# Optimization experiments

Measured on AMD Instinct MI355X. Metric: run time of the kernel, lower is better.

Reference implementation:

```python
import jax, jax.numpy as jnp
import numpy as np

H = 8  # heads hardcoded in LightGFormer


def layernorm(x, g, b, eps=1e-5):
    m = x.mean(-1, keepdims=True)
    v = ((x - m) ** 2).mean(-1, keepdims=True)
    return (x - m) / jnp.sqrt(v + eps) * g + b


def setup_inputs() -> dict:
    key = jax.random.key(0)
    B, N, D, L = 16, 512, 256, 4
    Dff = 4 * D
    ks = jax.random.split(key, 12)

    def w(k, shape, scale=0.02):
        return jax.random.normal(k, shape, jnp.float32) * scale

    return {
        "input": w(ks[0], (B, N, D), 1.0),
        "input_v": w(ks[1], (B, N, D), 1.0),
        "pos_emb": w(ks[2], (N, D)),
        "Wq": w(ks[3], (L, D, D)), "bq": jnp.zeros((L, D), jnp.float32),
        "Wk": w(ks[4], (L, D, D)), "bk": jnp.zeros((L, D), jnp.float32),
        "Wv": w(ks[5], (L, D, D)), "bv": jnp.zeros((L, D), jnp.float32),
        "Wo": w(ks[6], (L, D, D)), "bo": jnp.zeros((L, D), jnp.float32),
        "W1": w(ks[7], (L, D, Dff)), "b1": jnp.zeros((L, Dff), jnp.float32),
        "W2": w(ks[8], (L, Dff // 2, D // 2)), "b2": jnp.zeros((L, D // 2), jnp.float32),
        "g1": jnp.ones((L, D), jnp.float32), "be1": jnp.zeros((L, D), jnp.float32),
        "g2": jnp.ones((L, D), jnp.float32), "be2": jnp.zeros((L, D), jnp.float32),
        "gf": jnp.ones((D,), jnp.float32), "bf": jnp.zeros((D,), jnp.float32),
        "mask": jax.random.randint(ks[9], (N, N), 0, 2) > 0,
    }


def reference(input, input_v, pos_emb, Wq, bq, Wk, bk, Wv, bv, Wo, bo,
              W1, b1, W2, b2, g1, be1, g2, be2, gf, bf, mask):
    B, N, D = input.shape
    L = Wq.shape[0]
    dk = D // H
    scale = 1.0 / float(np.sqrt(dk))

    x = input + pos_emb[None]       # learned positional encoding
    xv = input_v + pos_emb[None]    # values stream (never updated across layers)

    for i in range(L):
        # --- self-attention: queries/keys from x, values from xv ---
        q = (x @ Wq[i] + bq[i]).reshape(B, N, H, dk)
        k = (x @ Wk[i] + bk[i]).reshape(B, N, H, dk)
        v = (xv @ Wv[i] + bv[i]).reshape(B, N, H, dk)
        att = jnp.einsum('bqhd,bkhd->bhqk', q, k) * scale
        if i % 2 == 1:  # odd layers use the mask (Lightformer alternation)
            att = jnp.where(mask[None, None], -jnp.inf, att)
        att = jax.nn.softmax(att, axis=-1)
        o = jnp.einsum('bhqk,bkhd->bqhd', att, v).reshape(B, N, D)
        o = o @ Wo[i] + bo[i]
        x = layernorm(x + o, g1[i], be1[i])
        # --- FFN with grouped second linear: [.., 2, 2D] @ [2D, D/2] ---
        h = jax.nn.gelu(x @ W1[i] + b1[i], approximate=False)
        h = (h.reshape(B, N, 2, 2 * D) @ W2[i] + b2[i]).reshape(B, N, D)
        x = layernorm(x + h, g2[i], be2[i])

    x = layernorm(x, gf, bf)  # final attention_norm
    return x
```

## Files before the change

### kernel.cpp

```cpp
#include <hip/hip_runtime.h>
#include <hip/hip_bf16.h>
#include <math.h>

#define BDIM 16
#define NSEQ 512
#define DMODEL 256
#define NLAYER 4
#define NHEAD 8
#define DK 32
#define DFF 1024
#define BN (BDIM * NSEQ)
#define ND (NSEQ * DMODEL)

typedef __bf16 bf16x8 __attribute__((ext_vector_type(8)));
typedef float floatx4 __attribute__((ext_vector_type(4)));
typedef unsigned uint32x2 __attribute__((ext_vector_type(2)));

static __device__ __forceinline__ unsigned short f2bf(float f) {
    unsigned u = __float_as_uint(f);
    unsigned r = (u + 0x7FFFu + ((u >> 16) & 1u)) >> 16;
    return (unsigned short)r;
}
static __device__ __forceinline__ float bf2f(unsigned short u) {
    return __uint_as_float(((unsigned)u) << 16);
}

static __device__ __forceinline__ void async_ld16(const unsigned short* g,
                                                  unsigned short* l) {
    __builtin_amdgcn_global_load_lds(
        (const __attribute__((address_space(1))) unsigned int*)g,
        (__attribute__((address_space(3))) unsigned int*)l, 16, 0, 0);
}

static __device__ __forceinline__ float gelu_f(float c) {
    float u = 0.7978845608028654f * (c + 0.044715f * c * c * c);
    return c * (1.f / (1.f + __expf(-2.f * u)));
}

static __device__ __forceinline__ unsigned cvtpk(float lo, float hi) {
    unsigned r;
    asm("v_cvt_pk_bf16_f32 %0, %1, %2" : "=v"(r) : "v"(lo), "v"(hi));
    return r;
}

static __device__ __forceinline__ size_t fd_addr(int tok, int col) {
    int panel = tok >> 4, l16 = tok & 15;
    int kt = col >> 5, kp = col & 31;
    int quad = (kp >> 2) & 3;
    int j = (kp & 3) + 4 * ((kp >> 4) & 1);
    return ((size_t)(panel * 8 + kt) << 9) + (l16 * 4 + quad) * 8 + j;
}

__global__ void conv_all_kernel(const float* __restrict__ Wq, const float* __restrict__ Wk,
                                const float* __restrict__ Wv, const float* __restrict__ Wo,
                                const float* __restrict__ W1, const float* __restrict__ W2,
                                const int* __restrict__ mask,
                                unsigned short* __restrict__ wq_s, unsigned short* __restrict__ wk_s,
                                unsigned short* __restrict__ wv_s,
                                unsigned short* __restrict__ wo_s,
                                unsigned short* __restrict__ w1_s, unsigned short* __restrict__ w2_s,
                                unsigned* __restrict__ bits) {
    int blk = blockIdx.x, tid = threadIdx.x;
    if (blk < 3072) {
        int i = blk * 256 + tid;
        int sel = i >> 18;
        int jj = i & 262143;
        int l = jj >> 16, o = jj & 65535;
        int j = o & 7, quad = (o >> 3) & 3, l16 = (o >> 5) & 15;
        int kt = (o >> 9) & 7, cg = (o >> 12) & 15;
        int k = kt * 32 + (j >> 2) * 16 + quad * 4 + (j & 3);
        int dout = cg * 16 + l16;
        const float* src = sel == 0 ? Wq : sel == 1 ? Wk : Wv;
        unsigned short* dst = sel == 0 ? wq_s : sel == 1 ? wk_s : wv_s;
        dst[(size_t)l * 65536 + o] = f2bf(src[(size_t)l * 65536 + k * 256 + dout]);
    } else if (blk < 4096) {
        int i = (blk - 3072) * 256 + tid;
        int l = i >> 16, o = i & 65535;
        int j = o & 7, quad = (o >> 3) & 3, l16 = (o >> 5) & 15;
        int kt = (o >> 9) & 7, cg = (o >> 12) & 15;
        int k = kt * 32 + (j >> 2) * 16 + quad * 4 + (j & 3);
        int dout = cg * 16 + l16;
        wo_s[(size_t)l * 65536 + o] = f2bf(Wo[(size_t)l * 65536 + k * 256 + dout]);
    } else if (blk < 8192) {
        int i = (blk - 4096) * 256 + tid;
        int l = i >> 18, o = i & 262143;
        int j = o & 7, quad = (o >> 3) & 3, l16 = (o >> 5) & 15;
        int kt = (o >> 9) & 7, cg = (o >> 12) & 63;
        int k = kt * 32 + (j >> 2) * 16 + quad * 4 + (j & 3);
        int dout = cg * 16 + l16;
        w1_s[(size_t)l * 262144 + o] = f2bf(W1[(size_t)l * 262144 + k * 1024 + dout]);
    } else if (blk < 9216) {
        int i = (blk - 8192) * 256 + tid;
        int l = i >> 16, o = i & 65535;
        int j = o & 7, quad = (o >> 3) & 3, l16 = (o >> 5) & 15;
        int kt = (o >> 9) & 15, cg = (o >> 13) & 7;
        int k = kt * 32 + (j >> 2) * 16 + quad * 4 + (j & 3);
        int dout = cg * 16 + l16;
        w2_s[(size_t)l * 65536 + o] = f2bf(W2[(size_t)l * 65536 + k * 128 + dout]);
    } else {
        int w = (blk - 9216) * 256 + tid;
        int r = w >> 4, wi = w & 15;
        const int* src = mask + r * NSEQ + wi * 32;
        unsigned acc = 0;
#pragma unroll
        for (int j = 0; j < 32; j++) acc |= (src[j] != 0 ? 1u : 0u) << j;
        bits[w] = acc;
    }
}

__global__ void add_pos_kernel(const float* __restrict__ in,
                               const float* __restrict__ inv,
                               const float* __restrict__ pos,
                               float* __restrict__ x,
                               unsigned short* __restrict__ xb,
                               unsigned short* __restrict__ xvb,
                               int total) {
    int i = blockIdx.x * blockDim.x + threadIdx.x;
    if (i < total) {
        float pe = pos[i % ND];
        float a = in[i] + pe;
        float b = inv[i] + pe;
        x[i] = a;
        size_t fa = fd_addr(i >> 8, i & 255);
        xb[fa] = f2bf(a);
        xvb[fa] = f2bf(b);
    }
}

__global__ __launch_bounds__(256) void qkv_mfma_kernel(
        const unsigned short* __restrict__ xb_f,
        const unsigned short* __restrict__ xvb_f,
        const unsigned short* __restrict__ wq_s, const unsigned short* __restrict__ wk_s,
        const unsigned short* __restrict__ wv_s,
        const float* __restrict__ bq, const float* __restrict__ bk,
        const float* __restrict__ bv,
        unsigned short* __restrict__ qo, unsigned short* __restrict__ ko,
        unsigned short* __restrict__ vo) {
    int bx = blockIdx.x;
    int proj = bx >> 9, panel = bx & 511;
    const unsigned short* A  = (proj == 2) ? xvb_f : xb_f;
    const unsigned short* W  = (proj == 0) ? wq_s : (proj == 1) ? wk_s : wv_s;
    const float* bias        = (proj == 0) ? bq  : (proj == 1) ? bk  : bv;
    unsigned short* Cb       = (proj == 0) ? qo  : (proj == 1) ? ko  : vo;
    float qscale = (proj == 0) ? 0.17677669529663687f : 1.f;

    int tid = threadIdx.x;
    int w = tid >> 6, lane = tid & 63, l16 = lane & 15, quad = lane >> 4;
    int fo = (l16 * 4 + quad) * 8;

    floatx4 acc[4];
#pragma unroll
    for (int cg = 0; cg < 4; cg++) acc[cg] = (floatx4)0.0f;

    bf16x8 afQ[4], bwQ[4][4];
#pragma unroll
    for (int p = 0; p < 4; p++) {
        afQ[p] = *(const bf16x8*)(A + ((size_t)panel * 8 + p) * 512 + fo);
#pragma unroll
        for (int cg = 0; cg < 4; cg++)
            bwQ[p][cg] = *(const bf16x8*)(W + ((size_t)((w * 4 + cg) * 8 + p)) * 512 + fo);
    }

#pragma unroll
    for (int kt = 0; kt < 8; kt++) {
        int sl = kt & 3;
#pragma unroll
        for (int cg = 0; cg < 4; cg++)
            acc[cg] = __builtin_amdgcn_mfma_f32_16x16x32_bf16(afQ[sl], bwQ[sl][cg], acc[cg], 0, 0, 0);
        if (kt < 4) {
            afQ[sl] = *(const bf16x8*)(A + ((size_t)panel * 8 + kt + 4) * 512 + fo);
#pragma unroll
            for (int cg = 0; cg < 4; cg++)
                bwQ[sl][cg] = *(const bf16x8*)(W + ((size_t)((w * 4 + cg) * 8 + kt + 4)) * 512 + fo);
        }
    }

#pragma unroll
    for (int cg = 0; cg < 4; cg++) {
        int gcol = w * 64 + cg * 16 + l16;
        float bb = bias[gcol];
#pragma unroll
        for (int r = 0; r < 4; r++) {
            int grow = panel * 16 + quad * 4 + r;
            float c = (acc[cg][r] + bb) * qscale;
            size_t off = ((size_t)((grow >> 9) * 8 + (gcol >> 5)) << 14)
                       + (size_t)(grow & 511) * 32 + (gcol & 31);
            Cb[off] = f2bf(c);
        }
    }
}

__global__ __launch_bounds__(512, 4) void ffn_fused_kernel(
        const unsigned short* __restrict__ ab_f,
        const unsigned short* __restrict__ wo_s,
        const unsigned short* __restrict__ w1_s,
        const unsigned short* __restrict__ w2_s,
        const float* __restrict__ bo,
        const float* __restrict__ g1, const float* __restrict__ be1,
        const float* __restrict__ b1,
        const float* __restrict__ b2,
        const float* __restrict__ g2, const float* __restrict__ be2,
        const float* __restrict__ gf, const float* __restrict__ bf_,
        float* __restrict__ xf, unsigned short* __restrict__ xb,
        float* __restrict__ outF, int finalize) {
    __shared__ unsigned short X1s[8 * 512];
    __shared__ unsigned short Hs[16 * 512];
    __shared__ float redA[16][8], redB[16][8];
    __shared__ float redC[16][8], redD[16][8];
    __shared__ float redE[16][8], redF[16][8];

    int tid = threadIdx.x;
    int w = tid >> 6, lane = tid & 63, l16 = lane & 15, quad = lane >> 4;
    int bid = blockIdx.x;
    int rowBase = bid * 16;
    int fo = (l16 * 4 + quad) * 8;

#define TR2(d0, d1, addr)                                                  \
    asm volatile("ds_read_b64_tr_b16 %0, %2\n\t"                           \
                 "ds_read_b64_tr_b16 %1, %2 offset:512"                    \
                 : "=&v"(d0), "=&v"(d1) : "v"(addr))

    float bo_r[2], g1_r[2], be1_r[2], g2_r[2], be2_r[2], gf_r[2], bfr_[2];
#pragma unroll
    for (int cg = 0; cg < 2; cg++) {
        int colA = w * 32 + cg * 16 + l16;
        bo_r[cg] = bo[colA]; g1_r[cg] = g1[colA]; be1_r[cg] = be1[colA];
        int colC = cg * 128 + w * 16 + l16;
        g2_r[cg] = g2[colC]; be2_r[cg] = be2[colC];
        gf_r[cg] = gf[colC]; bfr_[cg] = bf_[colC];
    }
    float b1_r[2][4];
#pragma unroll
    for (int g = 0; g < 2; g++)
#pragma unroll
        for (int c = 0; c < 4; c++)
            b1_r[g][c] = b1[g * 512 + w * 64 + c * 16 + l16];
    float b2_r = b2[w * 16 + l16];
    float x0r[4][2];
#pragma unroll
    for (int r = 0; r < 4; r++)
#pragma unroll
        for (int cg = 0; cg < 2; cg++)
            x0r[r][cg] = xf[(size_t)(rowBase + quad * 4 + r) * 256 + w * 32 + cg * 16 + l16];

    floatx4 accA[2];
    accA[0] = (floatx4)0.0f; accA[1] = (floatx4)0.0f;

    bf16x8 afQ[4], bwQ[4][2];
#pragma unroll
    for (int p = 0; p < 4; p++) {
        afQ[p] = *(const bf16x8*)(ab_f + ((size_t)bid * 8 + p) * 512 + fo);
#pragma unroll
        for (int cg = 0; cg < 2; cg++)
            bwQ[p][cg] = *(const bf16x8*)(wo_s + ((size_t)((w * 2 + cg) * 8 + p)) * 512 + fo);
    }

#pragma unroll
    for (int kt = 0; kt < 8; kt++) {
        int sl = kt & 3;
#pragma unroll
        for (int cg = 0; cg < 2; cg++)
            accA[cg] = __builtin_amdgcn_mfma_f32_16x16x32_bf16(afQ[sl], bwQ[sl][cg], accA[cg], 0, 0, 0);
        if (kt < 4) {
            afQ[sl] = *(const bf16x8*)(ab_f + ((size_t)bid * 8 + kt + 4) * 512 + fo);
#pragma unroll
            for (int cg = 0; cg < 2; cg++)
                bwQ[sl][cg] = *(const bf16x8*)(wo_s + ((size_t)((w * 2 + cg) * 8 + kt + 4)) * 512 + fo);
        }
    }

#pragma unroll
    for (int r = 0; r < 4; r++) {
        int tok = quad * 4 + r;
        float s = 0.f, s2 = 0.f;
#pragma unroll
        for (int cg = 0; cg < 2; cg++) {
            float v = accA[cg][r] + bo_r[cg] + x0r[r][cg];
            accA[cg][r] = v; s += v; s2 += v * v;
        }
#pragma unroll
        for (int off = 1; off <= 8; off <<= 1) {
            s += __shfl_xor(s, off);
            s2 += __shfl_xor(s2, off);
        }
        if (l16 == 0) { redA[tok][w] = s; redB[tok][w] = s2; }
    }
    __syncthreads();
#pragma unroll
    for (int r = 0; r < 4; r++) {
        int tok = quad * 4 + r;
        float ts = 0.f, tq = 0.f;
#pragma unroll
        for (int ww = 0; ww < 8; ww++) { ts += redA[tok][ww]; tq += redB[tok][ww]; }
        float mean = ts * (1.f / 256.f);
        float var = tq * (1.f / 256.f) - mean * mean;
        float rstd = rsqrtf(var + 1e-5f);
#pragma unroll
        for (int cg = 0; cg < 2; cg++)
            accA[cg][r] = (accA[cg][r] - mean) * rstd * g1_r[cg] + be1_r[cg];
    }
#pragma unroll
    for (int cg = 0; cg < 2; cg++) {
        uint32x2 pk;
        pk[0] = cvtpk(accA[cg][0], accA[cg][1]);
        pk[1] = cvtpk(accA[cg][2], accA[cg][3]);
        *(uint32x2*)&X1s[w * 512 + (cg * 16 + l16) * 16 + quad * 4] = pk;
    }
    __syncthreads();

    unsigned x1addr = (unsigned)(size_t)&X1s[0] + (unsigned)(lane * 8);
    unsigned haddr  = (unsigned)(size_t)&Hs[0]  + (unsigned)(lane * 8);

    floatx4 y[2];
    y[0] = (floatx4)0.0f; y[1] = (floatx4)0.0f;

#pragma unroll
    for (int g = 0; g < 2; g++) {
        floatx4 accB[4];
#pragma unroll
        for (int c = 0; c < 4; c++) accB[c] = (floatx4)0.0f;

        uint32x2 tA0, tA1, tB0, tB1;
        TR2(tA0, tA1, x1addr);
        TR2(tB0, tB1, x1addr + 1024u);
        bf16x8 bwB[2][4];
#pragma unroll
        for (int p = 0; p < 2; p++)
#pragma unroll
            for (int c = 0; c < 4; c++)
                bwB[p][c] = *(const bf16x8*)(w1_s +
                    ((size_t)((g * 32 + w * 4 + c) * 8 + p)) * 512 + fo);

#pragma unroll
        for (int kt = 0; kt < 8; kt++) {
            if (kt < 7) asm volatile("s_waitcnt lgkmcnt(2)");
            else        asm volatile("s_waitcnt lgkmcnt(0)");
            __builtin_amdgcn_sched_barrier(0);
            union { bf16x8 v8; uint32x2 u[2]; } afu;
            if ((kt & 1) == 0) { afu.u[0] = tA0; afu.u[1] = tA1; }
            else               { afu.u[0] = tB0; afu.u[1] = tB1; }
            if (kt < 6) {
                if ((kt & 1) == 0) TR2(tA0, tA1, x1addr + (unsigned)((kt + 2) * 1024));
                else               TR2(tB0, tB1, x1addr + (unsigned)((kt + 2) * 1024));
            }
            int sl = kt & 1;
#pragma unroll
            for (int c = 0; c < 4; c++)
                accB[c] = __builtin_amdgcn_mfma_f32_16x16x32_bf16(afu.v8, bwB[sl][c], accB[c], 0, 0, 0);
            if (kt < 6) {
#pragma unroll
                for (int c = 0; c < 4; c++)
                    bwB[sl][c] = *(const bf16x8*)(w1_s +
                        ((size_t)((g * 32 + w * 4 + c) * 8 + kt + 2)) * 512 + fo);
            }
        }
#pragma unroll
        for (int c = 0; c < 4; c++) {
            float bb = b1_r[g][c];
            float o0 = gelu_f(accB[c][0] + bb);
            float o1 = gelu_f(accB[c][1] + bb);
            float o2 = gelu_f(accB[c][2] + bb);
            float o3 = gelu_f(accB[c][3] + bb);
            int ct = w * 2 + (c >> 1), colL = (c & 1) * 16 + l16;
            uint32x2 pk;
            pk[0] = cvtpk(o0, o1);
            pk[1] = cvtpk(o2, o3);
            *(uint32x2*)&Hs[ct * 512 + colL * 16 + quad * 4] = pk;
        }
        __syncthreads();

        TR2(tA0, tA1, haddr);
        TR2(tB0, tB1, haddr + 1024u);
        bf16x8 bwC[4];
#pragma unroll
        for (int p = 0; p < 4; p++)
            bwC[p] = *(const bf16x8*)(w2_s + ((size_t)(w * 16 + p)) * 512 + fo);

#pragma unroll
        for (int kt = 0; kt < 16; kt++) {
            if (kt < 15) asm volatile("s_waitcnt lgkmcnt(2)");
            else         asm volatile("s_waitcnt lgkmcnt(0)");
            __builtin_amdgcn_sched_barrier(0);
            union { bf16x8 v8; uint32x2 u[2]; } afu;
            if ((kt & 1) == 0) { afu.u[0] = tA0; afu.u[1] = tA1; }
            else               { afu.u[0] = tB0; afu.u[1] = tB1; }
            if (kt < 14) {
                if ((kt & 1) == 0) TR2(tA0, tA1, haddr + (unsigned)((kt + 2) * 1024));
                else               TR2(tB0, tB1, haddr + (unsigned)((kt + 2) * 1024));
            }
            y[g] = __builtin_amdgcn_mfma_f32_16x16x32_bf16(afu.v8, bwC[kt & 3], y[g], 0, 0, 0);
            if (kt < 12)
                bwC[kt & 3] = *(const bf16x8*)(w2_s + ((size_t)(w * 16 + kt + 4)) * 512 + fo);
        }
        if (g == 0) __syncthreads();
    }
#undef TR2

#pragma unroll
    for (int r = 0; r < 4; r++) {
        int tok = quad * 4 + r;
        float s = 0.f, s2 = 0.f;
#pragma unroll
        for (int g = 0; g < 2; g++) {
            int col = g * 128 + w * 16 + l16;
            float x1v = bf2f(X1s[(col >> 5) * 512 + (col & 31) * 16 + tok]);
            float v = y[g][r] + b2_r + x1v;
            y[g][r] = v; s += v; s2 += v * v;
        }
#pragma unroll
        for (int off = 1; off <= 8; off <<= 1) {
            s += __shfl_xor(s, off);
            s2 += __shfl_xor(s2, off);
        }
        if (l16 == 0) { redC[tok][w] = s; redD[tok][w] = s2; }
    }
    __syncthreads();

    if (!finalize) {
#pragma unroll
        for (int r = 0; r < 4; r++) {
            int tok = quad * 4 + r;
            float ts = 0.f, tq = 0.f;
#pragma unroll
            for (int ww = 0; ww < 8; ww++) { ts += redC[tok][ww]; tq += redD[tok][ww]; }
            float mean = ts * (1.f / 256.f);
            float var = tq * (1.f / 256.f) - mean * mean;
            float rstd = rsqrtf(var + 1e-5f);
#pragma unroll
            for (int g = 0; g < 2; g++) {
                int col = g * 128 + w * 16 + l16;
                float o = (y[g][r] - mean) * rstd * g2_r[g] + be2_r[g];
                xf[(size_t)(rowBase + tok) * 256 + col] = o;
                xb[((size_t)(bid * 8 + (col >> 5)) << 9) + fd_addr(tok, col) % 512
                   + 0] = 0;
            }
        }
#pragma unroll
        for (int r = 0; r < 4; r++) {
            int tok = quad * 4 + r;
            float ts = 0.f, tq = 0.f;
#pragma unroll
            for (int ww = 0; ww < 8; ww++) { ts += redC[tok][ww]; tq += redD[tok][ww]; }
            float mean = ts * (1.f / 256.f);
            float var = tq * (1.f / 256.f) - mean * mean;
            float rstd = rsqrtf(var + 1e-5f);
#pragma unroll
            for (int g = 0; g < 2; g++) {
                int col = g * 128 + w * 16 + l16;
                float o = (y[g][r] - mean) * rstd * g2_r[g] + be2_r[g];
                int kp = col & 31;
                int qk = (kp >> 2) & 3, jk = (kp & 3) + 4 * ((kp >> 4) & 1);
                xb[((size_t)(bid * 8 + (col >> 5)) << 9) + (tok * 4 + qk) * 8 + jk] = f2bf(o);
            }
        }
    } else {
#pragma unroll
        for (int r = 0; r < 4; r++) {
            int tok = quad * 4 + r;
            float ts = 0.f, tq = 0.f;
#pragma unroll
            for (int ww = 0; ww < 8; ww++) { ts += redC[tok][ww]; tq += redD[tok][ww]; }
            float mean = ts * (1.f / 256.f);
            float var = tq * (1.f / 256.f) - mean * mean;
            float rstd = rsqrtf(var + 1e-5f);
            float s3 = 0.f, q3 = 0.f;
#pragma unroll
            for (int g = 0; g < 2; g++) {
                float o = (y[g][r] - mean) * rstd * g2_r[g] + be2_r[g];
                y[g][r] = o; s3 += o; q3 += o * o;
            }
#pragma unroll
            for (int off = 1; off <= 8; off <<= 1) {
                s3 += __shfl_xor(s3, off);
                q3 += __shfl_xor(q3, off);
            }
            if (l16 == 0) { redE[tok][w] = s3; redF[tok][w] = q3; }
        }
        __syncthreads();
#pragma unroll
        for (int r = 0; r < 4; r++) {
            int tok = quad * 4 + r;
            float ts = 0.f, tq = 0.f;
#pragma unroll
            for (int ww = 0; ww < 8; ww++) { ts += redE[tok][ww]; tq += redF[tok][ww]; }
            float mean = ts * (1.f / 256.f);
            float var = tq * (1.f / 256.f) - mean * mean;
            float rstd = rsqrtf(var + 1e-5f);
#pragma unroll
            for (int g = 0; g < 2; g++) {
                int col = g * 128 + w * 16 + l16;
                outF[(size_t)(rowBase + tok) * 256 + col]
                    = (y[g][r] - mean) * rstd * gf_r[g] + bfr_[g];
            }
        }
    }
}

__global__ __launch_bounds__(256, 4) void attn_mfma_kernel(
        const unsigned short* __restrict__ q, const unsigned short* __restrict__ k,
        const unsigned short* __restrict__ v, unsigned short* __restrict__ ab_f,
        const unsigned* __restrict__ mbits_g, int use_mask) {
    int bid = blockIdx.x;
    int qg = bid >> 7;
    int bh = bid & 127;
    int h = bh & 7, b = bh >> 3;
    int tid = threadIdx.x;

    __shared__ unsigned short Vs[2][NSEQ * 16];

    const unsigned short* kbase = k + (size_t)(b * 8 + h) * (NSEQ * DK);
    const unsigned short* vbase = v + (size_t)(b * 8 + h) * (NSEQ * DK);

#pragma unroll
    for (int db = 0; db < 2; db++) {
#pragma unroll
        for (int t = 0; t < 4; t++) {
            int c = t * 256 + tid;
            int kk = c >> 1, half = c & 1;
            async_ld16(vbase + (size_t)kk * 32 + db * 16 + half * 8,
                       &Vs[db][c * 8]);
        }
    }

    int wave = tid >> 6, lane = tid & 63, l16 = lane & 15, quad = lane >> 4;
    int qbase = qg * 64 + wave * 16;

    bf16x8 qf = *(const bf16x8*)(q + ((size_t)(b * 8 + h) * NSEQ + qbase + l16) * 32 + quad * 8);

    unsigned mw[16];
    if (use_mask) {
        const uint4* mr = (const uint4*)(mbits_g + (size_t)(qbase + l16) * 16);
#pragma unroll
        for (int w = 0; w < 4; w++) *(uint4*)&mw[w * 4] = mr[w];
    } else {
#pragma unroll
        for (int w = 0; w < 16; w++) mw[w] = 0;
    }
    __syncthreads();

    unsigned va0 = (unsigned)(size_t)&Vs[0][0] + (unsigned)(lane * 8);
    unsigned va1 = (unsigned)(size_t)&Vs[1][0] + (unsigned)(lane * 8);

    const unsigned short* kfrag = kbase + (size_t)l16 * DK + quad * 8;

    floatx4 oT0 = (floatx4)0.f, oT1 = (floatx4)0.f;
    float m_run = -INFINITY, l_part = 0.f;

    uint32x2 t00, t01, t02, t03, t10, t11, t12, t13;
#define TR_ISSUE8(cp)                                                      \
    asm volatile("ds_read_b64_tr_b16 %0, %8\n\t"                           \
                 "ds_read_b64_tr_b16 %1, %8 offset:512\n\t"                \
                 "ds_read_b64_tr_b16 %2, %8 offset:1024\n\t"               \
                 "ds_read_b64_tr_b16 %3, %8 offset:1536\n\t"               \
                 "ds_read_b64_tr_b16 %4, %9\n\t"                           \
                 "ds_read_b64_tr_b16 %5, %9 offset:512\n\t"                \
                 "ds_read_b64_tr_b16 %6, %9 offset:1024\n\t"               \
                 "ds_read_b64_tr_b16 %7, %9 offset:1536"                   \
                 : "=&v"(t00), "=&v"(t01), "=&v"(t02), "=&v"(t03),         \
                   "=&v"(t10), "=&v"(t11), "=&v"(t12), "=&v"(t13)          \
                 : "v"(va0 + (unsigned)((cp) * 2048)),                     \
                   "v"(va1 + (unsigned)((cp) * 2048)))
    TR_ISSUE8(0);

    bf16x8 k0 = *(const bf16x8*)(kfrag);
    bf16x8 k1 = *(const bf16x8*)(kfrag + 16 * DK);
    bf16x8 k2 = *(const bf16x8*)(kfrag + 32 * DK);
    bf16x8 k3 = *(const bf16x8*)(kfrag + 48 * DK);

#pragma unroll
    for (int cp = 0; cp < 8; cp++) {
        floatx4 s0 = __builtin_amdgcn_mfma_f32_16x16x32_bf16(k0, qf, (floatx4)0.f, 0, 0, 0);
        floatx4 s1 = __builtin_amdgcn_mfma_f32_16x16x32_bf16(k1, qf, (floatx4)0.f, 0, 0, 0);
        floatx4 s2 = __builtin_amdgcn_mfma_f32_16x16x32_bf16(k2, qf, (floatx4)0.f, 0, 0, 0);
        floatx4 s3 = __builtin_amdgcn_mfma_f32_16x16x32_bf16(k3, qf, (floatx4)0.f, 0, 0, 0);

        bf16x8 k0n, k1n, k2n, k3n;
        if (cp < 7) {
            const unsigned short* kn = kfrag + (size_t)((cp + 1) * 64) * DK;
            k0n = *(const bf16x8*)(kn);
            k1n = *(const bf16x8*)(kn + 16 * DK);
            k2n = *(const bf16x8*)(kn + 32 * DK);
            k3n = *(const bf16x8*)(kn + 48 * DK);
        }

        float sv[16];
#pragma unroll
        for (int r = 0; r < 4; r++) {
            sv[r] = s0[r]; sv[4 + r] = s1[r];
            sv[8 + r] = s2[r]; sv[12 + r] = s3[r];
        }
        if (use_mask) {
            unsigned wb0 = mw[2 * cp], wb1 = mw[2 * cp + 1];
#pragma unroll
            for (int r = 0; r < 4; r++) {
                if ((wb0 >> (quad * 4 + r)) & 1)        sv[r]      = -INFINITY;
                if ((wb0 >> (16 + quad * 4 + r)) & 1)   sv[4 + r]  = -INFINITY;
                if ((wb1 >> (quad * 4 + r)) & 1)        sv[8 + r]  = -INFINITY;
                if ((wb1 >> (16 + quad * 4 + r)) & 1)   sv[12 + r] = -INFINITY;
            }
        }
        float mx = sv[0];
#pragma unroll
        for (int j = 1; j < 16; j++) mx = fmaxf(mx, sv[j]);
        mx = fmaxf(mx, __shfl_xor(mx, 16));
        mx = fmaxf(mx, __shfl_xor(mx, 32));
        if (!__all(mx <= m_run)) {
            float mnew = fmaxf(m_run, mx);
            float corr = (m_run == mnew) ? 1.f : __expf(m_run - mnew);
            l_part *= corr;
            oT0 *= corr; oT1 *= corr;
            m_run = mnew;
        }
        float p[16];
#pragma unroll
        for (int j = 0; j < 16; j++) {
            float e = __expf(sv[j] - m_run);
            p[j] = (sv[j] > -INFINITY) ? e : 0.f;
            l_part += p[j];
        }
        union { bf16x8 v8; unsigned u[4]; } pf0, pf1;
#pragma unroll
        for (int j = 0; j < 4; j++) {
            pf0.u[j] = cvtpk(p[2 * j], p[2 * j + 1]);
            pf1.u[j] = cvtpk(p[8 + 2 * j], p[8 + 2 * j + 1]);
        }

        asm volatile("s_waitcnt lgkmcnt(0)");
        __builtin_amdgcn_sched_barrier(0);
        union { bf16x8 v8; uint32x2 u[2]; } av0, av1, av2, av3;
        av0.u[0] = t00; av0.u[1] = t01;
        av2.u[0] = t02; av2.u[1] = t03;
        av1.u[0] = t10; av1.u[1] = t11;
        av3.u[0] = t12; av3.u[1] = t13;

        oT0 = __builtin_amdgcn_mfma_f32_16x16x32_bf16(av0.v8, pf0.v8, oT0, 0, 0, 0);
        oT1 = __builtin_amdgcn_mfma_f32_16x16x32_bf16(av1.v8, pf0.v8, oT1, 0, 0, 0);
        oT0 = __builtin_amdgcn_mfma_f32_16x16x32_bf16(av2.v8, pf1.v8, oT0, 0, 0, 0);
        oT1 = __builtin_amdgcn_mfma_f32_16x16x32_bf16(av3.v8, pf1.v8, oT1, 0, 0, 0);
        if (cp < 7) TR_ISSUE8(cp + 1);
        k0 = k0n; k1 = k1n; k2 = k2n; k3 = k3n;
    }
#undef TR_ISSUE8

    float l = l_part;
    l += __shfl_xor(l, 16);
    l += __shfl_xor(l, 32);
    float invl = (l > 0.f) ? 1.f / l : 0.f;

    uint4 val;
    val.x = cvtpk(oT0[0] * invl, oT0[1] * invl);
    val.y = cvtpk(oT0[2] * invl, oT0[3] * invl);
    val.z = cvtpk(oT1[0] * invl, oT1[1] * invl);
    val.w = cvtpk(oT1[2] * invl, oT1[3] * invl);
    size_t panel = (size_t)b * 32 + qg * 4 + wave;
    *(uint4*)(ab_f + (panel * 8 + h) * 512 + (l16 * 4 + quad) * 8) = val;
}

extern "C" void kernel_launch(void* const* d_in, const int* in_sizes, int n_in,
                              void* d_out, int out_size, void* d_ws, size_t ws_size,
                              hipStream_t stream) {
    const float* input  = (const float*)d_in[0];
    const float* inputv = (const float*)d_in[1];
    const float* pos    = (const float*)d_in[2];
    const float* Wq = (const float*)d_in[3];
    const float* bq = (const float*)d_in[4];
    const float* Wk = (const float*)d_in[5];
    const float* bk = (const float*)d_in[6];
    const float* Wv = (const float*)d_in[7];
    const float* bv = (const float*)d_in[8];
    const float* Wo = (const float*)d_in[9];
    const float* bo = (const float*)d_in[10];
    const float* W1 = (const float*)d_in[11];
    const float* b1 = (const float*)d_in[12];
    const float* W2 = (const float*)d_in[13];
    const float* b2 = (const float*)d_in[14];
    const float* g1 = (const float*)d_in[15];
    const float* be1 = (const float*)d_in[16];
    const float* g2 = (const float*)d_in[17];
    const float* be2 = (const float*)d_in[18];
    const float* gf = (const float*)d_in[19];
    const float* bff = (const float*)d_in[20];
    const int* mask = (const int*)d_in[21];

    float* out = (float*)d_out;

    char* wsb = (char*)d_ws;
    float* x_f  = (float*)(wsb + ((size_t)0 << 20));
    unsigned short* x_b  = (unsigned short*)(wsb + ((size_t)8 << 20));
    unsigned short* xv_b = (unsigned short*)(wsb + ((size_t)12 << 20));
    unsigned short* qb_b = (unsigned short*)(wsb + ((size_t)16 << 20));
    unsigned short* kb_b = (unsigned short*)(wsb + ((size_t)20 << 20));
    unsigned short* vb_b = (unsigned short*)(wsb + ((size_t)24 << 20));
    unsigned short* ab_f = (unsigned short*)(wsb + ((size_t)28 << 20));
    unsigned short* wq_s = (unsigned short*)(wsb + ((size_t)32 << 20));
    unsigned short* wk_s = wq_s + (size_t)4 * 65536;
    unsigned short* wv_s = wk_s + (size_t)4 * 65536;
    unsigned short* wo_s = wv_s + (size_t)4 * 65536;
    unsigned short* w1_s = wo_s + (size_t)4 * 65536;
    unsigned short* w2_s = w1_s + (size_t)4 * 262144;
    unsigned* mbits = (unsigned*)(wsb + ((size_t)37 << 20));

    const size_t TOK = (size_t)BN * DMODEL;

    conv_all_kernel<<<9248, 256, 0, stream>>>(Wq, Wk, Wv, Wo, W1, W2, mask,
                                              wq_s, wk_s, wv_s, wo_s, w1_s, w2_s, mbits);
    add_pos_kernel<<<(int)((TOK + 255) / 256), 256, 0, stream>>>(
        input, inputv, pos, x_f, x_b, xv_b, (int)TOK);

    for (int i = 0; i < NLAYER; i++) {
        const unsigned short* Wq_i = wq_s + (size_t)i * 65536;
        const unsigned short* Wk_i = wk_s + (size_t)i * 65536;
        const unsigned short* Wv_i = wv_s + (size_t)i * 65536;
        const unsigned short* Wo_i = wo_s + (size_t)i * 65536;
        const unsigned short* W1_i = w1_s + (size_t)i * 262144;
        const unsigned short* W2_i = w2_s + (size_t)i * 65536;

        qkv_mfma_kernel<<<1536, 256, 0, stream>>>(
            x_b, xv_b, Wq_i, Wk_i, Wv_i,
            bq + i * DMODEL, bk + i * DMODEL, bv + i * DMODEL,
            qb_b, kb_b, vb_b);

        attn_mfma_kernel<<<BDIM * NHEAD * 8, 256, 0, stream>>>(
            qb_b, kb_b, vb_b, ab_f, mbits, (i & 1));

        ffn_fused_kernel<<<BN / 16, 512, 0, stream>>>(
            ab_f, Wo_i, W1_i, W2_i,
            bo + i * DMODEL, g1 + i * DMODEL, be1 + i * DMODEL,
            b1 + i * DFF, b2 + i * (DMODEL / 2),
            g2 + i * DMODEL, be2 + i * DMODEL,
            gf, bff, x_f, x_b, out, (i == NLAYER - 1) ? 1 : 0);
    }
}
```

Before: 406.9 us.

## Retile QKV projection to 64-row by 128-column blocks and drop redundant zero stores

The QKV projection kernel now gives each block 4 row panels and half of the output columns, with each wave computing 4x2 MFMA tiles. This lets each loaded weight fragment be reused across four row panels. The K loop is software-pipelined with next-step prefetch registers, and the grid is halved. Separately, the FFN epilogue no longer writes zeros to the bf16 activation buffer and then recomputes the layernorm in a second pass; it writes the final bf16 value in the same loop. This trades higher register use and fewer blocks for less global load traffic and fewer stores.

```diff
diff --git a/kernel.cpp b/kernel.cpp
--- a/kernel.cpp
+++ b/kernel.cpp
@@ -137,7 +137,8 @@
         unsigned short* __restrict__ qo, unsigned short* __restrict__ ko,
         unsigned short* __restrict__ vo) {
     int bx = blockIdx.x;
-    int proj = bx >> 9, panel = bx & 511;
+    int proj = bx >> 8, rem = bx & 255;
+    int tg = rem >> 1, ch = rem & 1;
     const unsigned short* A  = (proj == 2) ? xvb_f : xb_f;
     const unsigned short* W  = (proj == 0) ? wq_s : (proj == 1) ? wk_s : wv_s;
     const float* bias        = (proj == 0) ? bq  : (proj == 1) ? bk  : bv;
@@ -148,44 +149,58 @@
     int w = tid >> 6, lane = tid & 63, l16 = lane & 15, quad = lane >> 4;
     int fo = (l16 * 4 + quad) * 8;
 
-    floatx4 acc[4];
-#pragma unroll
-    for (int cg = 0; cg < 4; cg++) acc[cg] = (floatx4)0.0f;
-
-    bf16x8 afQ[4], bwQ[4][4];
-#pragma unroll
-    for (int p = 0; p < 4; p++) {
-        afQ[p] = *(const bf16x8*)(A + ((size_t)panel * 8 + p) * 512 + fo);
-#pragma unroll
-        for (int cg = 0; cg < 4; cg++)
-            bwQ[p][cg] = *(const bf16x8*)(W + ((size_t)((w * 4 + cg) * 8 + p)) * 512 + fo);
-    }
+    floatx4 acc[4][2];
+#pragma unroll
+    for (int pp = 0; pp < 4; pp++)
+#pragma unroll
+        for (int cg = 0; cg < 2; cg++) acc[pp][cg] = (floatx4)0.0f;
+
+    bf16x8 af[4], afn[4], bw[2], bwn[2];
+#pragma unroll
+    for (int pp = 0; pp < 4; pp++)
+        af[pp] = *(const bf16x8*)(A + ((size_t)(tg * 4 + pp) * 8 + 0) * 512 + fo);
+#pragma unroll
+    for (int cg = 0; cg < 2; cg++)
+        bw[cg] = *(const bf16x8*)(W + ((size_t)((ch * 8 + w * 2 + cg) * 8 + 0)) * 512 + fo);
 
 #pragma unroll
     for (int kt = 0; kt < 8; kt++) {
-        int sl = kt & 3;
-#pragma unroll
-        for (int cg = 0; cg < 4; cg++)
-            acc[cg] = __builtin_amdgcn_mfma_f32_16x16x32_bf16(afQ[sl], bwQ[sl][cg], acc[cg], 0, 0, 0);
-        if (kt < 4) {
-            afQ[sl] = *(const bf16x8*)(A + ((size_t)panel * 8 + kt + 4) * 512 + fo);
-#pragma unroll
-            for (int cg = 0; cg < 4; cg++)
-                bwQ[sl][cg] = *(const bf16x8*)(W + ((size_t)((w * 4 + cg) * 8 + kt + 4)) * 512 + fo);
-        }
-    }
-
-#pragma unroll
-    for (int cg = 0; cg < 4; cg++) {
-        int gcol = w * 64 + cg * 16 + l16;
+        if (kt < 7) {
+#pragma unroll
+            for (int pp = 0; pp < 4; pp++)
+                afn[pp] = *(const bf16x8*)(A + ((size_t)(tg * 4 + pp) * 8 + kt + 1) * 512 + fo);
+#pragma unroll
+            for (int cg = 0; cg < 2; cg++)
+                bwn[cg] = *(const bf16x8*)(W + ((size_t)((ch * 8 + w * 2 + cg) * 8 + kt + 1)) * 512 + fo);
+        }
+#pragma unroll
+        for (int pp = 0; pp < 4; pp++)
+#pragma unroll
+            for (int cg = 0; cg < 2; cg++)
+                acc[pp][cg] = __builtin_amdgcn_mfma_f32_16x16x32_bf16(
+                    af[pp], bw[cg], acc[pp][cg], 0, 0, 0);
+        if (kt < 7) {
+#pragma unroll
+            for (int pp = 0; pp < 4; pp++) af[pp] = afn[pp];
+#pragma unroll
+            for (int cg = 0; cg < 2; cg++) bw[cg] = bwn[cg];
+        }
+    }
+
+#pragma unroll
+    for (int cg = 0; cg < 2; cg++) {
+        int gcol = ch * 128 + w * 32 + cg * 16 + l16;
         float bb = bias[gcol];
 #pragma unroll
-        for (int r = 0; r < 4; r++) {
-            int grow = panel * 16 + quad * 4 + r;
-            float c = (acc[cg][r] + bb) * qscale;
-            size_t off = ((size_t)((grow >> 9) * 8 + (gcol >> 5)) << 14)
-                       + (size_t)(grow & 511) * 32 + (gcol & 31);
-            Cb[off] = f2bf(c);
+        for (int pp = 0; pp < 4; pp++) {
+#pragma unroll
+            for (int r = 0; r < 4; r++) {
+                int grow = (tg * 4 + pp) * 16 + quad * 4 + r;
+                float c = (acc[pp][cg][r] + bb) * qscale;
+                size_t off = ((size_t)((grow >> 9) * 8 + (gcol >> 5)) << 14)
+                           + (size_t)(grow & 511) * 32 + (gcol & 31);
+                Cb[off] = f2bf(c);
+            }
         }
     }
 }
@@ -431,23 +446,6 @@
                 int col = g * 128 + w * 16 + l16;
                 float o = (y[g][r] - mean) * rstd * g2_r[g] + be2_r[g];
                 xf[(size_t)(rowBase + tok) * 256 + col] = o;
-                xb[((size_t)(bid * 8 + (col >> 5)) << 9) + fd_addr(tok, col) % 512
-                   + 0] = 0;
-            }
-        }
-#pragma unroll
-        for (int r = 0; r < 4; r++) {
-            int tok = quad * 4 + r;
-            float ts = 0.f, tq = 0.f;
-#pragma unroll
-            for (int ww = 0; ww < 8; ww++) { ts += redC[tok][ww]; tq += redD[tok][ww]; }
-            float mean = ts * (1.f / 256.f);
-            float var = tq * (1.f / 256.f) - mean * mean;
-            float rstd = rsqrtf(var + 1e-5f);
-#pragma unroll
-            for (int g = 0; g < 2; g++) {
-                int col = g * 128 + w * 16 + l16;
-                float o = (y[g][r] - mean) * rstd * g2_r[g] + be2_r[g];
                 int kp = col & 31;
                 int qk = (kp >> 2) & 3, jk = (kp & 3) + 4 * ((kp >> 4) & 1);
                 xb[((size_t)(bid * 8 + (col >> 5)) << 9) + (tok * 4 + qk) * 8 + jk] = f2bf(o);
@@ -715,7 +713,7 @@
         const unsigned short* W1_i = w1_s + (size_t)i * 262144;
         const unsigned short* W2_i = w2_s + (size_t)i * 65536;
 
-        qkv_mfma_kernel<<<1536, 256, 0, stream>>>(
+        qkv_mfma_kernel<<<768, 256, 0, stream>>>(
             x_b, xv_b, Wq_i, Wk_i, Wv_i,
             bq + i * DMODEL, bk + i * DMODEL, bv + i * DMODEL,
             qb_b, kb_b, vb_b);
```

New measurement: 385.4 us. 5.3% less time.
